# Kernel tuning notes

Hardware: AMD Instinct MI355X
Metric: run time of the kernel (lower is better)

Reference implementation:

```python
import jax, jax.numpy as jnp
import numpy as np
from jax.ops import segment_sum, segment_max

N = 50000      # nodes
E = 600000     # edges
D_IN = 128     # input_dim
H = 128        # hidden_dim
OUT = 32       # output_dim (classes)
G = 50         # graphs in batch
HEADS = 2


def setup_inputs() -> dict:
    key = jax.random.key(0)
    ks = jax.random.split(key, 16)
    s = 0.05
    inp = {
        "x": jax.random.normal(ks[0], (N, D_IN), jnp.float32),
        "edge_index": jax.random.randint(ks[1], (2, E), 0, N, dtype=jnp.int64),
        "batch": jnp.sort(jax.random.randint(ks[2], (N,), 0, G, dtype=jnp.int64)),
        # GCN layers: weight [in, out] (applied as x @ W), bias [out]
        "W1": jax.random.normal(ks[3], (D_IN, H), jnp.float32) * s,
        "b1": jnp.zeros((H,), jnp.float32),
        "W2": jax.random.normal(ks[4], (H, H), jnp.float32) * s,
        "b2": jnp.zeros((H,), jnp.float32),
        "W3": jax.random.normal(ks[5], (H, H), jnp.float32) * s,
        "b3": jnp.zeros((H,), jnp.float32),
        # GAT: lin weight [H, HEADS*H], attention vecs [HEADS, H], bias [H] (concat=False)
        "gat_W": jax.random.normal(ks[6], (H, HEADS * H), jnp.float32) * s,
        "att_src": jax.random.normal(ks[7], (HEADS, H), jnp.float32) * s,
        "att_dst": jax.random.normal(ks[8], (HEADS, H), jnp.float32) * s,
        "gat_b": jnp.zeros((H,), jnp.float32),
        # MLP head
        "fc1_W": jax.random.normal(ks[9], (H, H), jnp.float32) * s,
        "fc1_b": jnp.zeros((H,), jnp.float32),
        "fc2_W": jax.random.normal(ks[10], (H, OUT), jnp.float32) * s,
        "fc2_b": jnp.zeros((OUT,), jnp.float32),
    }
    return inp


def _add_self_loops(src, dst, n):
    loop = jnp.arange(n, dtype=src.dtype)
    return jnp.concatenate([src, loop]), jnp.concatenate([dst, loop])


def _gcn_conv(x, W, b, src, dst, n):
    # PyG GCNConv: self-loops + symmetric normalization deg^-1/2 A deg^-1/2
    h = x @ W                                  # [N, H]
    deg = segment_sum(jnp.ones_like(dst, dtype=h.dtype), dst, num_segments=n)
    dinv = jnp.where(deg > 0, jax.lax.rsqrt(deg), 0.0)
    norm = dinv[src] * dinv[dst]               # [E']
    out = segment_sum(h[src] * norm[:, None], dst, num_segments=n)
    return out + b


def _gat_conv(x, W, a_src, a_dst, b, src, dst, n):
    # PyG GATConv, heads=HEADS, concat=False (mean over heads), self-loops added
    h = (x @ W).reshape(n, HEADS, -1)          # [N, heads, H]
    al_s = jnp.einsum('nhc,hc->nh', h, a_src)  # [N, heads]
    al_d = jnp.einsum('nhc,hc->nh', h, a_dst)
    alpha = jax.nn.leaky_relu(al_s[src] + al_d[dst], 0.2)   # [E', heads]
    m = segment_max(alpha, dst, num_segments=n)             # per-dst max
    ea = jnp.exp(alpha - m[dst])
    denom = segment_sum(ea, dst, num_segments=n)
    coef = ea / (denom[dst] + 1e-16)                         # [E', heads]
    out = segment_sum(h[src] * coef[:, :, None], dst, num_segments=n)  # [N, heads, H]
    return out.mean(axis=1) + b


def reference(x, edge_index, batch, W1, b1, W2, b2, W3, b3,
              gat_W, att_src, att_dst, gat_b, fc1_W, fc1_b, fc2_W, fc2_b):
    n = x.shape[0]
    src, dst = _add_self_loops(edge_index[0], edge_index[1], n)
    h = jax.nn.relu(_gcn_conv(x, W1, b1, src, dst, n))
    h = jax.nn.relu(_gcn_conv(h, W2, b2, src, dst, n))
    h = jax.nn.relu(_gcn_conv(h, W3, b3, src, dst, n))
    h = jax.nn.relu(_gat_conv(h, gat_W, att_src, att_dst, gat_b, src, dst, n))
    # pooling: mean + add share the same segment sum
    sums = segment_sum(h, batch, num_segments=G)             # [G, H]
    counts = segment_sum(jnp.ones((n,), h.dtype), batch, num_segments=G)
    g = sums / jnp.maximum(counts, 1.0)[:, None] + sums
    g = jax.nn.relu(g @ fc1_W + fc1_b)
    logits = g @ fc2_W + fc2_b
    return jax.nn.log_softmax(logits, axis=1)
```

## Files before the change

### kernel.cpp

```cpp
#include <hip/hip_runtime.h>
#include <hip/hip_bf16.h>

typedef __attribute__((ext_vector_type(8))) short short8v;
typedef __attribute__((ext_vector_type(4))) float float4v;
typedef __attribute__((ext_vector_type(2))) float f32x2;

__device__ __forceinline__ unsigned short f2bf(float f) {
    unsigned u = __float_as_uint(f);
    u += 0x7FFFu + ((u >> 16) & 1u);
    return (unsigned short)(u >> 16);
}
__device__ __forceinline__ float bflo(unsigned u) { return __uint_as_float(u << 16); }
__device__ __forceinline__ float bfhi(unsigned u) { return __uint_as_float(u & 0xFFFF0000u); }
__device__ __forceinline__ float lrelu02(float a) { return (a > 0.f) ? a : 0.2f * a; }
__device__ __forceinline__ unsigned pack2(float a, float b) {
    return (unsigned)f2bf(a) | ((unsigned)f2bf(b) << 16);
}

__global__ void setup_kernel(const float* __restrict__ W1, const float* __restrict__ W2,
                             const float* __restrict__ W3, const float* __restrict__ WG,
                             unsigned short* __restrict__ Wt1, unsigned short* __restrict__ Wt2,
                             unsigned short* __restrict__ Wt3, unsigned short* __restrict__ WtG,
                             int* __restrict__ deg, float* __restrict__ sums,
                             float* __restrict__ cnts, int N, int G) {
    int idx = blockIdx.x * blockDim.x + threadIdx.x;
    if (idx < 16384) {
        int i = idx;           int k = i >> 7, n = i & 127;  Wt1[n * 128 + k] = f2bf(W1[i]);
    } else if (idx < 32768) {
        int i = idx - 16384;   int k = i >> 7, n = i & 127;  Wt2[n * 128 + k] = f2bf(W2[i]);
    } else if (idx < 49152) {
        int i = idx - 32768;   int k = i >> 7, n = i & 127;  Wt3[n * 128 + k] = f2bf(W3[i]);
    } else if (idx < 81920) {
        int i = idx - 49152;   int k = i >> 8, n = i & 255;  WtG[n * 128 + k] = f2bf(WG[i]);
    } else if (idx < 81920 + N) {
        deg[idx - 81920] = 0;
    } else if (idx < 81920 + N + G * 128) {
        sums[idx - 81920 - N] = 0.f;
    } else if (idx < 81920 + N + G * 128 + G) {
        cnts[idx - 81920 - N - G * 128] = 0.f;
    }
}


__global__ void deg_kernel(const int* __restrict__ dst, int* __restrict__ deg, int E) {
    int i = blockIdx.x * blockDim.x + threadIdx.x;
    if (i < E) atomicAdd(&deg[dst[i]], 1);
}

__global__ __launch_bounds__(1024) void scan_kernel(const int* __restrict__ deg,
                                                    int* __restrict__ ptr,
                                                    int* __restrict__ cursor,
                                                    float* __restrict__ dinv, int N) {
    __shared__ int wsum[16];
    const int tid = threadIdx.x, wid = tid >> 6, lane = tid & 63;
    int carry = 0;
    for (int base = 0; base < N; base += 1024) {
        int i = base + tid;
        int v = (i < N) ? deg[i] : 0;
        int x = v;
#pragma unroll
        for (int o = 1; o < 64; o <<= 1) {
            int t = __shfl_up(x, o);
            if (lane >= o) x += t;
        }
        if (lane == 63) wsum[wid] = x;
        __syncthreads();
        if (wid == 0 && lane < 16) {
            int w = wsum[lane];
#pragma unroll
            for (int o = 1; o < 16; o <<= 1) {
                int t = __shfl_up(w, o);
                if (lane >= o) w += t;
            }
            wsum[lane] = w;
        }
        __syncthreads();
        int excl = carry + (wid ? wsum[wid - 1] : 0) + x - v;
        if (i < N) {
            ptr[i] = excl; cursor[i] = excl;
            dinv[i] = rsqrtf((float)v + 1.0f);
        }
        carry += wsum[15];
        __syncthreads();
    }
    if (tid == 0) ptr[N] = carry;
}

__global__ void csr_fill_kernel(const int* __restrict__ src, const int* __restrict__ dst,
                                int* __restrict__ cursor, int* __restrict__ csr_src, int E) {
    int e = blockIdx.x * blockDim.x + threadIdx.x;
    if (e < E) {
        int pos = atomicAdd(&cursor[dst[e]], 1);
        csr_src[pos] = src[e];
    }
}

template<bool XF32>
__global__ __launch_bounds__(256) void lin_mfma_kernel(const void* __restrict__ Xv,
                                                       const unsigned short* __restrict__ Wt,
                                                       const float* __restrict__ dinv,
                                                       unsigned short* __restrict__ Y, int N) {
    constexpr int NF = 8;
    int wave = threadIdx.x >> 6;
    int lane = threadIdx.x & 63;
    int lr = lane & 15;
    int hk = lane >> 4;
    int rowbase = blockIdx.x * 64 + wave * 16;
    int arow = rowbase + lr; if (arow > N - 1) arow = N - 1;
    float4v acc[NF];
#pragma unroll
    for (int i = 0; i < NF; ++i) acc[i] = (float4v){0.f, 0.f, 0.f, 0.f};
#pragma unroll
    for (int ks = 0; ks < 4; ++ks) {
        int k0 = ks * 32 + hk * 8;
        short8v a;
        if (XF32) {
            const float* xp = (const float*)Xv + (size_t)arow * 128 + k0;
            float4 a0 = *(const float4*)xp;
            float4 a1 = *(const float4*)(xp + 4);
            a[0] = (short)f2bf(a0.x); a[1] = (short)f2bf(a0.y);
            a[2] = (short)f2bf(a0.z); a[3] = (short)f2bf(a0.w);
            a[4] = (short)f2bf(a1.x); a[5] = (short)f2bf(a1.y);
            a[6] = (short)f2bf(a1.z); a[7] = (short)f2bf(a1.w);
        } else {
            a = *(const short8v*)((const unsigned short*)Xv + (size_t)arow * 128 + k0);
        }
#pragma unroll
        for (int nf = 0; nf < NF; ++nf) {
            short8v b = *(const short8v*)(Wt + (size_t)(nf * 16 + lr) * 128 + k0);
            acc[nf] = __builtin_amdgcn_mfma_f32_16x16x32_bf16(a, b, acc[nf], 0, 0, 0);
        }
    }
#pragma unroll
    for (int r = 0; r < 4; ++r) {
        int orow = rowbase + hk * 4 + r;
        if (orow < N) {
            float scale = dinv[orow];
            unsigned short* yp = Y + (size_t)orow * 128 + lr;
#pragma unroll
            for (int nf = 0; nf < NF; ++nf) yp[nf * 16] = f2bf(acc[nf][r] * scale);
        }
    }
}

__global__ __launch_bounds__(256) void lin_mfma_attn_kernel(const unsigned short* __restrict__ X,
                                                            const unsigned short* __restrict__ Wt,
                                                            const float* __restrict__ attS,
                                                            const float* __restrict__ attD,
                                                            uint2* __restrict__ Yf8,
                                                            float2* __restrict__ al_s2,
                                                            float2* __restrict__ al_d2, int N) {
    constexpr int NF = 16;
    int wave = threadIdx.x >> 6;
    int lane = threadIdx.x & 63;
    int lr = lane & 15;
    int hk = lane >> 4;
    int rowbase = blockIdx.x * 64 + wave * 16;
    int arow = rowbase + lr; if (arow > N - 1) arow = N - 1;
    float4v acc[NF];
#pragma unroll
    for (int i = 0; i < NF; ++i) acc[i] = (float4v){0.f, 0.f, 0.f, 0.f};
#pragma unroll
    for (int ks = 0; ks < 4; ++ks) {
        int k0 = ks * 32 + hk * 8;
        short8v a = *(const short8v*)(X + (size_t)arow * 128 + k0);
#pragma unroll
        for (int nf = 0; nf < NF; ++nf) {
            short8v b = *(const short8v*)(Wt + (size_t)(nf * 16 + lr) * 128 + k0);
            acc[nf] = __builtin_amdgcn_mfma_f32_16x16x32_bf16(a, b, acc[nf], 0, 0, 0);
        }
    }
    float as0[8], as1[8], ad0[8], ad1[8];
#pragma unroll
    for (int q = 0; q < 8; ++q) {
        as0[q] = attS[q * 16 + lr];
        as1[q] = attS[128 + q * 16 + lr];
        ad0[q] = attD[q * 16 + lr];
        ad1[q] = attD[128 + q * 16 + lr];
    }
#pragma unroll
    for (int r = 0; r < 4; ++r) {
        int orow = rowbase + hk * 4 + r;
        float s0 = 0.f, s1 = 0.f, d0 = 0.f, d1 = 0.f;
#pragma unroll
        for (int q = 0; q < 8; ++q) {
            s0 += acc[q][r] * as0[q];
            d0 += acc[q][r] * ad0[q];
            s1 += acc[q + 8][r] * as1[q];
            d1 += acc[q + 8][r] * ad1[q];
        }
#pragma unroll
        for (int o = 1; o < 16; o <<= 1) {
            s0 += __shfl_xor(s0, o);
            s1 += __shfl_xor(s1, o);
            d0 += __shfl_xor(d0, o);
            d1 += __shfl_xor(d1, o);
        }
        if (orow < N) {
            int w0 = __builtin_amdgcn_cvt_pk_fp8_f32(acc[0][r], acc[1][r], 0, 0);
            w0 = __builtin_amdgcn_cvt_pk_fp8_f32(acc[2][r], acc[3][r], w0, 1);
            int w1 = __builtin_amdgcn_cvt_pk_fp8_f32(acc[4][r], acc[5][r], 0, 0);
            w1 = __builtin_amdgcn_cvt_pk_fp8_f32(acc[6][r], acc[7][r], w1, 1);
            Yf8[(size_t)orow * 32 + lr] = make_uint2((unsigned)w0, (unsigned)w1);
            int w2 = __builtin_amdgcn_cvt_pk_fp8_f32(acc[8][r], acc[9][r], 0, 0);
            w2 = __builtin_amdgcn_cvt_pk_fp8_f32(acc[10][r], acc[11][r], w2, 1);
            int w3 = __builtin_amdgcn_cvt_pk_fp8_f32(acc[12][r], acc[13][r], 0, 0);
            w3 = __builtin_amdgcn_cvt_pk_fp8_f32(acc[14][r], acc[15][r], w3, 1);
            Yf8[(size_t)orow * 32 + 16 + lr] = make_uint2((unsigned)w2, (unsigned)w3);
            if (lr == 0) {
                al_s2[orow] = make_float2(s0, s1);
                al_d2[orow] = make_float2(d0, d1);
            }
        }
    }
}

__global__ __launch_bounds__(256) void gcn_gather_kernel(const uint4* __restrict__ y,
                                                         const float* __restrict__ dinv,
                                                         const int* __restrict__ ptr,
                                                         const int* __restrict__ csr,
                                                         const float* __restrict__ bias,
                                                         uint4* __restrict__ out, int N) {
    __shared__ int stg[4][64];
    int w = threadIdx.x >> 6;
    int node = blockIdx.x * 4 + w;
    if (node >= N) return;
    int lane = threadIdx.x & 63;
    int q = lane & 15;
    int g = lane >> 4;
    float a0 = 0.f, a1 = 0.f, a2 = 0.f, a3 = 0.f, a4 = 0.f, a5 = 0.f, a6 = 0.f, a7 = 0.f;
    int b0 = ptr[node], b1 = ptr[node + 1];
    for (int p0 = b0; p0 < b1; p0 += 64) {
        int m = b1 - p0; if (m > 64) m = 64;
        if (lane < m) stg[w][lane] = __builtin_nontemporal_load(csr + p0 + lane);
        int j = g;
        for (; j + 4 < m; j += 8) {
            int s0 = stg[w][j], s1 = stg[w][j + 4];
            uint4 u0 = y[(size_t)s0 * 16 + q];
            uint4 u1 = y[(size_t)s1 * 16 + q];
            a0 += bflo(u0.x) + bflo(u1.x); a1 += bfhi(u0.x) + bfhi(u1.x);
            a2 += bflo(u0.y) + bflo(u1.y); a3 += bfhi(u0.y) + bfhi(u1.y);
            a4 += bflo(u0.z) + bflo(u1.z); a5 += bfhi(u0.z) + bfhi(u1.z);
            a6 += bflo(u0.w) + bflo(u1.w); a7 += bfhi(u0.w) + bfhi(u1.w);
        }
        if (j < m) {
            int s0 = stg[w][j];
            uint4 u0 = y[(size_t)s0 * 16 + q];
            a0 += bflo(u0.x); a1 += bfhi(u0.x);
            a2 += bflo(u0.y); a3 += bfhi(u0.y);
            a4 += bflo(u0.z); a5 += bfhi(u0.z);
            a6 += bflo(u0.w); a7 += bfhi(u0.w);
        }
    }
#pragma unroll
    for (int o = 16; o < 64; o <<= 1) {
        a0 += __shfl_xor(a0, o); a1 += __shfl_xor(a1, o);
        a2 += __shfl_xor(a2, o); a3 += __shfl_xor(a3, o);
        a4 += __shfl_xor(a4, o); a5 += __shfl_xor(a5, o);
        a6 += __shfl_xor(a6, o); a7 += __shfl_xor(a7, o);
    }
    uint4 su = y[(size_t)node * 16 + q];
    a0 += bflo(su.x); a1 += bfhi(su.x);
    a2 += bflo(su.y); a3 += bfhi(su.y);
    a4 += bflo(su.z); a5 += bfhi(su.z);
    a6 += bflo(su.w); a7 += bfhi(su.w);
    if (lane < 16) {
        float dn = dinv[node];
        float4 bb0 = *(const float4*)(bias + q * 8);
        float4 bb1 = *(const float4*)(bias + q * 8 + 4);
        a0 = fmaxf(a0 * dn + bb0.x, 0.f); a1 = fmaxf(a1 * dn + bb0.y, 0.f);
        a2 = fmaxf(a2 * dn + bb0.z, 0.f); a3 = fmaxf(a3 * dn + bb0.w, 0.f);
        a4 = fmaxf(a4 * dn + bb1.x, 0.f); a5 = fmaxf(a5 * dn + bb1.y, 0.f);
        a6 = fmaxf(a6 * dn + bb1.z, 0.f); a7 = fmaxf(a7 * dn + bb1.w, 0.f);
        out[(size_t)node * 16 + q] = make_uint4(pack2(a0, a1), pack2(a2, a3),
                                                pack2(a4, a5), pack2(a6, a7));
    }
}

__global__ __launch_bounds__(256) void gat_gather_kernel(const uint2* __restrict__ h2,
                                                         const float2* __restrict__ al_s2,
                                                         const float2* __restrict__ al_d2,
                                                         const int* __restrict__ ptr,
                                                         const int* __restrict__ csr,
                                                         const float* __restrict__ bias,
                                                         uint4* __restrict__ out, int N) {
    __shared__ uint4 stg[4][64];
    __shared__ float vals[4][128];
    int w = threadIdx.x >> 6;
    int node = blockIdx.x * 4 + w;
    if (node >= N) return;
    int lane = threadIdx.x & 63;
    int li = lane & 31;
    int head = li >> 4;
    int g = lane >> 5;
    int b0 = ptr[node], b1 = ptr[node + 1];
    float2 ad = al_d2[node];

    float den0 = 0.f, den1 = 0.f;
    float a0 = 0.f, a1 = 0.f, a2 = 0.f, a3 = 0.f, a4 = 0.f, a5 = 0.f, a6 = 0.f, a7 = 0.f;

    for (int p0 = b0; p0 < b1; p0 += 64) {
        int m = b1 - p0; if (m > 64) m = 64;
        int idx = (lane < m) ? __builtin_nontemporal_load(csr + p0 + lane) : 0;
        float2 als = al_s2[idx];
        float e0 = __expf(lrelu02(als.x + ad.x));
        float e1 = __expf(lrelu02(als.y + ad.y));
        if (lane >= m) { e0 = 0.f; e1 = 0.f; }
        den0 += e0; den1 += e1;
        stg[w][lane] = make_uint4((unsigned)idx, __float_as_uint(e0), __float_as_uint(e1), 0u);
        int j = g;
        for (; j + 2 < m; j += 4) {
            uint4 t0 = stg[w][j], t1 = stg[w][j + 2];
            uint2 u0 = h2[(size_t)t0.x * 32 + li];
            uint2 u1 = h2[(size_t)t1.x * 32 + li];
            float c0 = __uint_as_float(head ? t0.z : t0.y);
            float c1 = __uint_as_float(head ? t1.z : t1.y);
            f32x2 p0v = __builtin_amdgcn_cvt_pk_f32_fp8(u0.x, 0);
            f32x2 p1v = __builtin_amdgcn_cvt_pk_f32_fp8(u0.x, 1);
            f32x2 p2v = __builtin_amdgcn_cvt_pk_f32_fp8(u0.y, 0);
            f32x2 p3v = __builtin_amdgcn_cvt_pk_f32_fp8(u0.y, 1);
            f32x2 q0v = __builtin_amdgcn_cvt_pk_f32_fp8(u1.x, 0);
            f32x2 q1v = __builtin_amdgcn_cvt_pk_f32_fp8(u1.x, 1);
            f32x2 q2v = __builtin_amdgcn_cvt_pk_f32_fp8(u1.y, 0);
            f32x2 q3v = __builtin_amdgcn_cvt_pk_f32_fp8(u1.y, 1);
            a0 += p0v[0] * c0 + q0v[0] * c1; a1 += p0v[1] * c0 + q0v[1] * c1;
            a2 += p1v[0] * c0 + q1v[0] * c1; a3 += p1v[1] * c0 + q1v[1] * c1;
            a4 += p2v[0] * c0 + q2v[0] * c1; a5 += p2v[1] * c0 + q2v[1] * c1;
            a6 += p3v[0] * c0 + q3v[0] * c1; a7 += p3v[1] * c0 + q3v[1] * c1;
        }
        if (j < m) {
            uint4 t0 = stg[w][j];
            uint2 u0 = h2[(size_t)t0.x * 32 + li];
            float c0 = __uint_as_float(head ? t0.z : t0.y);
            f32x2 p0v = __builtin_amdgcn_cvt_pk_f32_fp8(u0.x, 0);
            f32x2 p1v = __builtin_amdgcn_cvt_pk_f32_fp8(u0.x, 1);
            f32x2 p2v = __builtin_amdgcn_cvt_pk_f32_fp8(u0.y, 0);
            f32x2 p3v = __builtin_amdgcn_cvt_pk_f32_fp8(u0.y, 1);
            a0 += p0v[0] * c0; a1 += p0v[1] * c0;
            a2 += p1v[0] * c0; a3 += p1v[1] * c0;
            a4 += p2v[0] * c0; a5 += p2v[1] * c0;
            a6 += p3v[0] * c0; a7 += p3v[1] * c0;
        }
    }
    a0 += __shfl_xor(a0, 32); a1 += __shfl_xor(a1, 32);
    a2 += __shfl_xor(a2, 32); a3 += __shfl_xor(a3, 32);
    a4 += __shfl_xor(a4, 32); a5 += __shfl_xor(a5, 32);
    a6 += __shfl_xor(a6, 32); a7 += __shfl_xor(a7, 32);
#pragma unroll
    for (int o = 1; o < 64; o <<= 1) {
        den0 += __shfl_xor(den0, o);
        den1 += __shfl_xor(den1, o);
    }
    {
        float2 as_ = al_s2[node];
        float e0s = __expf(lrelu02(as_.x + ad.x));
        float e1s = __expf(lrelu02(as_.y + ad.y));
        den0 += e0s; den1 += e1s;
        float ea = head ? e1s : e0s;
        uint2 u = h2[(size_t)node * 32 + li];
        f32x2 p0v = __builtin_amdgcn_cvt_pk_f32_fp8(u.x, 0);
        f32x2 p1v = __builtin_amdgcn_cvt_pk_f32_fp8(u.x, 1);
        f32x2 p2v = __builtin_amdgcn_cvt_pk_f32_fp8(u.y, 0);
        f32x2 p3v = __builtin_amdgcn_cvt_pk_f32_fp8(u.y, 1);
        a0 += ea * p0v[0]; a1 += ea * p0v[1];
        a2 += ea * p1v[0]; a3 += ea * p1v[1];
        a4 += ea * p2v[0]; a5 += ea * p2v[1];
        a6 += ea * p3v[0]; a7 += ea * p3v[1];
    }
    float inv = 1.f / ((head ? den1 : den0) + 1e-16f);
    a0 *= inv; a1 *= inv; a2 *= inv; a3 *= inv;
    a4 *= inv; a5 *= inv; a6 *= inv; a7 *= inv;
    a0 += __shfl_xor(a0, 16); a1 += __shfl_xor(a1, 16);
    a2 += __shfl_xor(a2, 16); a3 += __shfl_xor(a3, 16);
    a4 += __shfl_xor(a4, 16); a5 += __shfl_xor(a5, 16);
    a6 += __shfl_xor(a6, 16); a7 += __shfl_xor(a7, 16);
    if (lane < 16) {
        vals[w][lane * 8 + 0] = a0; vals[w][lane * 8 + 1] = a1;
        vals[w][lane * 8 + 2] = a2; vals[w][lane * 8 + 3] = a3;
        vals[w][lane * 8 + 4] = a4; vals[w][lane * 8 + 5] = a5;
        vals[w][lane * 8 + 6] = a6; vals[w][lane * 8 + 7] = a7;
    }
    if (lane < 16) {
        float o[8];
#pragma unroll
        for (int i = 0; i < 8; ++i) {
            int c = lane * 8 + i;
            int p = (c & 15) * 8 + (c >> 4);
            o[i] = fmaxf(0.5f * vals[w][p] + bias[c], 0.f);
        }
        out[(size_t)node * 16 + lane] = make_uint4(pack2(o[0], o[1]), pack2(o[2], o[3]),
                                                   pack2(o[4], o[5]), pack2(o[6], o[7]));
    }
}

__global__ __launch_bounds__(256) void pool_kernel(const unsigned* __restrict__ h,
                                                   const int* __restrict__ batch,
                                                   float* __restrict__ sums,
                                                   float* __restrict__ counts, int N) {
    const int PER = 32;
    int wave = threadIdx.x >> 6;
    int f = threadIdx.x & 63;
    int n0 = (blockIdx.x * 4 + wave) * PER;
    int n1 = min(N, n0 + PER);
    if (n0 >= n1) return;
    int cur = -1;
    float a0 = 0.f, a1 = 0.f, cnt = 0.f;
    for (int n = n0; n < n1; ++n) {
        int g = batch[n];
        if (g != cur) {
            if (cur >= 0) {
                atomicAdd(&sums[cur * 128 + f * 2], a0);
                atomicAdd(&sums[cur * 128 + f * 2 + 1], a1);
                if (f == 0) atomicAdd(&counts[cur], cnt);
            }
            cur = g; a0 = a1 = cnt = 0.f;
        }
        unsigned u = h[(size_t)n * 64 + f];
        a0 += bflo(u); a1 += bfhi(u); cnt += 1.f;
    }
    if (cur >= 0) {
        atomicAdd(&sums[cur * 128 + f * 2], a0);
        atomicAdd(&sums[cur * 128 + f * 2 + 1], a1);
        if (f == 0) atomicAdd(&counts[cur], cnt);
    }
}

__global__ __launch_bounds__(128) void head_kernel(const float* __restrict__ sums,
                                                   const float* __restrict__ counts,
                                                   const float* __restrict__ fc1W,
                                                   const float* __restrict__ fc1b,
                                                   const float* __restrict__ fc2W,
                                                   const float* __restrict__ fc2b,
                                                   float* __restrict__ out) {
    int g = blockIdx.x;
    int tid = threadIdx.x;
    __shared__ float gm[128];
    __shared__ float h1[128];
    __shared__ float part[4][32];
    float s = sums[g * 128 + tid];
    gm[tid] = s / fmaxf(counts[g], 1.f) + s;
    __syncthreads();
    float acc = fc1b[tid];
    for (int k = 0; k < 128; ++k) acc += gm[k] * fc1W[k * 128 + tid];
    h1[tid] = fmaxf(acc, 0.f);
    __syncthreads();
    int c = tid & 31, p = tid >> 5;
    float a2 = 0.f;
    for (int k = p * 32; k < p * 32 + 32; ++k) a2 += h1[k] * fc2W[k * 32 + c];
    part[p][c] = a2;
    __syncthreads();
    if (tid < 32) {
        float v = part[0][tid] + part[1][tid] + part[2][tid] + part[3][tid] + fc2b[tid];
        float m = v;
#pragma unroll
        for (int o = 1; o < 32; o <<= 1) m = fmaxf(m, __shfl_xor(m, o));
        float e = __expf(v - m);
        float ssum = e;
#pragma unroll
        for (int o = 1; o < 32; o <<= 1) ssum += __shfl_xor(ssum, o);
        out[g * 32 + tid] = v - m - logf(ssum);
    }
}


extern "C" void kernel_launch(void* const* d_in, const int* in_sizes, int n_in,
                              void* d_out, int out_size, void* d_ws, size_t ws_size,
                              hipStream_t stream) {
    const float* x     = (const float*)d_in[0];
    const int*   eidx  = (const int*)d_in[1];
    const int*   batch = (const int*)d_in[2];
    const float* W1 = (const float*)d_in[3];
    const float* b1 = (const float*)d_in[4];
    const float* W2 = (const float*)d_in[5];
    const float* b2 = (const float*)d_in[6];
    const float* W3 = (const float*)d_in[7];
    const float* b3 = (const float*)d_in[8];
    const float* gatW   = (const float*)d_in[9];
    const float* attSrc = (const float*)d_in[10];
    const float* attDst = (const float*)d_in[11];
    const float* gatB   = (const float*)d_in[12];
    const float* fc1W = (const float*)d_in[13];
    const float* fc1b = (const float*)d_in[14];
    const float* fc2W = (const float*)d_in[15];
    const float* fc2b = (const float*)d_in[16];
    float* out = (float*)d_out;

    const int N  = in_sizes[0] / 128;
    const int E  = in_sizes[1] / 2;
    const int OUT = in_sizes[15] / 128;
    const int G   = out_size / OUT;

    const int* src = eidx;
    const int* dst = eidx + E;

    char* ws = (char*)d_ws;
    size_t off = 0;
    auto carve = [&](size_t bytes) { char* p = ws + off; off += (bytes + 255) & ~255ull; return p; };
    unsigned short* yb   = (unsigned short*)carve((size_t)N * 128 * 2);
    unsigned short* hb   = (unsigned short*)carve((size_t)N * 128 * 2);
    uint2*          gb8  = (uint2*)carve((size_t)N * 256);
    unsigned short* Wt1 = (unsigned short*)carve(128 * 128 * 2);
    unsigned short* Wt2 = (unsigned short*)carve(128 * 128 * 2);
    unsigned short* Wt3 = (unsigned short*)carve(128 * 128 * 2);
    unsigned short* WtG = (unsigned short*)carve(256 * 128 * 2);
    int*   deg   = (int*)carve((size_t)N * 4);
    float* dinv  = (float*)carve((size_t)N * 4);
    int*   ptr   = (int*)carve((size_t)(N + 1) * 4);
    int*   cursor= (int*)carve((size_t)N * 4);
    int*   csrS  = (int*)carve((size_t)E * 4);
    float* al_s  = (float*)carve((size_t)N * 2 * 4);
    float* al_d  = (float*)carve((size_t)N * 2 * 4);
    float* sums  = (float*)carve((size_t)G * 128 * 4);
    float* cnts  = (float*)carve((size_t)G * 4);

    const int B = 256;
    dim3 blk(B);
    auto cdiv = [](long long a, long long b) { return (int)((a + b - 1) / b); };

    setup_kernel<<<cdiv(81920 + N + G * 128 + G, B), blk, 0, stream>>>(
        W1, W2, W3, gatW, Wt1, Wt2, Wt3, WtG, deg, sums, cnts, N, G);

    deg_kernel<<<cdiv(E, B), blk, 0, stream>>>(dst, deg, E);
    scan_kernel<<<1, 1024, 0, stream>>>(deg, ptr, cursor, dinv, N);
    csr_fill_kernel<<<cdiv(E, B), blk, 0, stream>>>(src, dst, cursor, csrS, E);

    lin_mfma_kernel<true><<<cdiv(N, 64), blk, 0, stream>>>(x, Wt1, dinv, yb, N);
    gcn_gather_kernel<<<cdiv(N, 4), blk, 0, stream>>>((const uint4*)yb, dinv, ptr, csrS, b1, (uint4*)hb, N);
    lin_mfma_kernel<false><<<cdiv(N, 64), blk, 0, stream>>>(hb, Wt2, dinv, yb, N);
    gcn_gather_kernel<<<cdiv(N, 4), blk, 0, stream>>>((const uint4*)yb, dinv, ptr, csrS, b2, (uint4*)hb, N);
    lin_mfma_kernel<false><<<cdiv(N, 64), blk, 0, stream>>>(hb, Wt3, dinv, yb, N);
    gcn_gather_kernel<<<cdiv(N, 4), blk, 0, stream>>>((const uint4*)yb, dinv, ptr, csrS, b3, (uint4*)hb, N);

    lin_mfma_attn_kernel<<<cdiv(N, 64), blk, 0, stream>>>(hb, WtG, attSrc, attDst, gb8,
                                                          (float2*)al_s, (float2*)al_d, N);
    gat_gather_kernel<<<cdiv(N, 4), blk, 0, stream>>>(gb8, (const float2*)al_s, (const float2*)al_d,
                                                      ptr, csrS, gatB, (uint4*)yb, N);

    pool_kernel<<<cdiv(N, 128), blk, 0, stream>>>((const unsigned*)yb, batch, sums, cnts, N);

    head_kernel<<<G, dim3(128), 0, stream>>>(sums, cnts, fc1W, fc1b, fc2W, fc2b, out);
}
```

Measured before the change: 372.7 us.

## Split single-block degree scan into multi-block two-pass scan

Replaces the single-workgroup serial loop over all nodes with a two-pass scan. The first pass computes per-block local prefix sums and block totals across many workgroups, and the second adds block offsets and writes the cursor. This removes a serialized single-CU kernel of about 49 iterations with barriers, at the cost of one extra kernel launch and a small bsum buffer limited to 256 blocks.

Result: faster. 329.2 us (-11.7%).

```diff
diff --git a/kernel.cpp b/kernel.cpp
--- a/kernel.cpp
+++ b/kernel.cpp
@@ -47,43 +47,62 @@
     if (i < E) atomicAdd(&deg[dst[i]], 1);
 }
 
-__global__ __launch_bounds__(1024) void scan_kernel(const int* __restrict__ deg,
-                                                    int* __restrict__ ptr,
-                                                    int* __restrict__ cursor,
-                                                    float* __restrict__ dinv, int N) {
+__global__ __launch_bounds__(1024) void scan1_kernel(const int* __restrict__ deg,
+                                                     int* __restrict__ ptr,
+                                                     float* __restrict__ dinv,
+                                                     int* __restrict__ bsum, int N) {
     __shared__ int wsum[16];
     const int tid = threadIdx.x, wid = tid >> 6, lane = tid & 63;
-    int carry = 0;
-    for (int base = 0; base < N; base += 1024) {
-        int i = base + tid;
-        int v = (i < N) ? deg[i] : 0;
-        int x = v;
-#pragma unroll
-        for (int o = 1; o < 64; o <<= 1) {
-            int t = __shfl_up(x, o);
-            if (lane >= o) x += t;
-        }
-        if (lane == 63) wsum[wid] = x;
-        __syncthreads();
-        if (wid == 0 && lane < 16) {
-            int w = wsum[lane];
-#pragma unroll
-            for (int o = 1; o < 16; o <<= 1) {
-                int t = __shfl_up(w, o);
-                if (lane >= o) w += t;
-            }
-            wsum[lane] = w;
-        }
-        __syncthreads();
-        int excl = carry + (wid ? wsum[wid - 1] : 0) + x - v;
-        if (i < N) {
-            ptr[i] = excl; cursor[i] = excl;
-            dinv[i] = rsqrtf((float)v + 1.0f);
-        }
-        carry += wsum[15];
-        __syncthreads();
-    }
-    if (tid == 0) ptr[N] = carry;
+    int i = blockIdx.x * 1024 + tid;
+    int v = (i < N) ? deg[i] : 0;
+    int x = v;
+#pragma unroll
+    for (int o = 1; o < 64; o <<= 1) {
+        int t = __shfl_up(x, o);
+        if (lane >= o) x += t;
+    }
+    if (lane == 63) wsum[wid] = x;
+    __syncthreads();
+    if (wid == 0 && lane < 16) {
+        int w = wsum[lane];
+#pragma unroll
+        for (int o = 1; o < 16; o <<= 1) {
+            int t = __shfl_up(w, o);
+            if (lane >= o) w += t;
+        }
+        wsum[lane] = w;
+    }
+    __syncthreads();
+    int excl = (wid ? wsum[wid - 1] : 0) + x - v;
+    if (i < N) {
+        ptr[i] = excl;
+        dinv[i] = rsqrtf((float)v + 1.0f);
+    }
+    if (tid == 0) bsum[blockIdx.x] = wsum[15];
+}
+
+__global__ __launch_bounds__(1024) void scan2_kernel(int* __restrict__ ptr,
+                                                     int* __restrict__ cursor,
+                                                     const int* __restrict__ bsum,
+                                                     int N, int nb) {
+    __shared__ int offs;
+    const int tid = threadIdx.x;
+    if (tid < 64) {
+        int s = 0;
+        for (int j = (int)tid; j < (int)blockIdx.x; j += 64) s += bsum[j];
+#pragma unroll
+        for (int o = 1; o < 64; o <<= 1) s += __shfl_xor(s, o);
+        if (tid == 0) offs = s;
+    }
+    __syncthreads();
+    int off = offs;
+    int i = blockIdx.x * 1024 + tid;
+    if (i < N) {
+        int v = ptr[i] + off;
+        ptr[i] = v;
+        cursor[i] = v;
+    }
+    if ((int)blockIdx.x == nb - 1 && tid == 0) ptr[N] = off + bsum[nb - 1];
 }
 
 __global__ void csr_fill_kernel(const int* __restrict__ src, const int* __restrict__ dst,
@@ -508,6 +527,7 @@
     int*   ptr   = (int*)carve((size_t)(N + 1) * 4);
     int*   cursor= (int*)carve((size_t)N * 4);
     int*   csrS  = (int*)carve((size_t)E * 4);
+    int*   bsum  = (int*)carve(256 * 4);
     float* al_s  = (float*)carve((size_t)N * 2 * 4);
     float* al_d  = (float*)carve((size_t)N * 2 * 4);
     float* sums  = (float*)carve((size_t)G * 128 * 4);
@@ -516,12 +536,14 @@
     const int B = 256;
     dim3 blk(B);
     auto cdiv = [](long long a, long long b) { return (int)((a + b - 1) / b); };
+    const int nb = cdiv(N, 1024);
 
     setup_kernel<<<cdiv(81920 + N + G * 128 + G, B), blk, 0, stream>>>(
         W1, W2, W3, gatW, Wt1, Wt2, Wt3, WtG, deg, sums, cnts, N, G);
 
     deg_kernel<<<cdiv(E, B), blk, 0, stream>>>(dst, deg, E);
-    scan_kernel<<<1, 1024, 0, stream>>>(deg, ptr, cursor, dinv, N);
+    scan1_kernel<<<nb, 1024, 0, stream>>>(deg, ptr, dinv, bsum, N);
+    scan2_kernel<<<nb, 1024, 0, stream>>>(ptr, cursor, bsum, N, nb);
     csr_fill_kernel<<<cdiv(E, B), blk, 0, stream>>>(src, dst, cursor, csrS, E);
 
     lin_mfma_kernel<true><<<cdiv(N, 64), blk, 0, stream>>>(x, Wt1, dinv, yb, N);
```
